# Performance work log

Measured on AMD Instinct MI355X. Metric: run time of the kernel, lower is better.

The kernel has to match this reference:

```python
import jax, jax.numpy as jnp
import numpy as np

N = 50000      # nodes
E = 1600000    # edges (avg degree 32)
IN = 4         # in_size
H = 64         # hidden size


def _gcn_conv(x, W, b, src, dst, ew, n):
    """PyG GCNConv with edge_weight: add self-loops (weight 1), symmetric
    deg^{-1/2} normalization, gather-transform-scatter aggregation, then bias."""
    xw = x @ W  # [n, out] transform first (PyG lin before propagate)
    loops = jnp.arange(n)
    s = jnp.concatenate([src, loops])
    d = jnp.concatenate([dst, loops])
    w = jnp.concatenate([ew, jnp.ones((n,), ew.dtype)])
    deg = jax.ops.segment_sum(w, d, num_segments=n)
    dinv = jnp.where(deg > 0, jax.lax.rsqrt(deg), 0.0)
    norm = dinv[s] * w * dinv[d]                      # [E+n]
    msg = xw[s] * norm[:, None]                       # [E+n, out]
    out = jax.ops.segment_sum(msg, d, num_segments=n)
    return out + b


def _tower(x, src, dst, ew, W0, b0, W1, b1, W2, b2, Wl, bl):
    # basic_gcn: GCNConv+ReLU, GCNConv+ReLU, GCNConv, then nn.Linear(out,out)
    n = x.shape[0]
    h = jax.nn.relu(_gcn_conv(x, W0, b0, src, dst, ew, n))
    h = jax.nn.relu(_gcn_conv(h, W1, b1, src, dst, ew, n))
    h = _gcn_conv(h, W2, b2, src, dst, ew, n)
    return h @ Wl + bl


def setup_inputs() -> dict:
    key = jax.random.key(0)
    ks = jax.random.split(key, 20)
    x = jax.random.normal(ks[0], (N, IN), dtype=jnp.float32)
    edge_index = jax.random.randint(ks[1], (2, E), 0, N, dtype=jnp.int64)
    edge_weights = jax.random.uniform(ks[2], (E,), dtype=jnp.float32)

    def lin(k, fin, fout):
        return jax.random.normal(k, (fin, fout), dtype=jnp.float32) * (1.0 / np.sqrt(fin))

    inp = {"x": x, "edge_index": edge_index, "edge_weights": edge_weights}
    # optim tower: in_size=4 -> 64 -> 64 -> 1, plus Linear(1,1)
    inp["o_W0"], inp["o_b0"] = lin(ks[3], IN, H), jnp.zeros((H,), jnp.float32)
    inp["o_W1"], inp["o_b1"] = lin(ks[4], H, H), jnp.zeros((H,), jnp.float32)
    inp["o_W2"], inp["o_b2"] = lin(ks[5], H, 1), jnp.zeros((1,), jnp.float32)
    inp["o_Wl"], inp["o_bl"] = lin(ks[6], 1, 1), jnp.zeros((1,), jnp.float32)
    # gamma tower: in_size+1=5 -> 64 -> 64 -> 1, plus Linear(1,1)
    inp["g_W0"], inp["g_b0"] = lin(ks[7], IN + 1, H), jnp.zeros((H,), jnp.float32)
    inp["g_W1"], inp["g_b1"] = lin(ks[8], H, H), jnp.zeros((H,), jnp.float32)
    inp["g_W2"], inp["g_b2"] = lin(ks[9], H, 1), jnp.zeros((1,), jnp.float32)
    inp["g_Wl"], inp["g_bl"] = lin(ks[10], 1, 1), jnp.zeros((1,), jnp.float32)
    return inp


def reference(x, edge_index, edge_weights,
              o_W0, o_b0, o_W1, o_b1, o_W2, o_b2, o_Wl, o_bl,
              g_W0, g_b0, g_W1, g_b1, g_W2, g_b2, g_Wl, g_bl):
    src, dst = edge_index[0], edge_index[1]
    # x_sol = optim tower (constraints=None -> no range scaling)
    x_sol = _tower(x, src, dst, edge_weights,
                   o_W0, o_b0, o_W1, o_b1, o_W2, o_b2, o_Wl, o_bl)  # [N,1]
    # gamma tower on cat(x, x_sol[:, -1:]); constraints=[0,1] -> sigmoid scaling
    xin = jnp.concatenate([x, x_sol[:, -1:]], axis=1)               # [N,5]
    g = _tower(xin, src, dst, edge_weights,
               g_W0, g_b0, g_W1, g_b1, g_W2, g_b2, g_Wl, g_bl)      # [N,1]
    gamma = jax.nn.sigmoid(g)  # scale_to_range(x, [0,1])
    # s == g == 1: gated residual combine
    x_new = x[:, -1:] + gamma * (x_sol - x[:, -1:])
    return (x_new, gamma)
```

## Files before the change

kernel.cpp:

```cpp
#include <hip/hip_runtime.h>
#include <hip/hip_fp16.h>
#include <math.h>

#define NN 50000
#define NE 1600000
#define NBK 196
#define EPB 4096
#define CAP 9216

typedef unsigned int u32;
typedef _Float16 f16x8 __attribute__((ext_vector_type(8)));
typedef float f32x4 __attribute__((ext_vector_type(4)));

static inline int cdiv(int a, int b){ return (a + b - 1) / b; }



__global__ void k_bucket(const int* __restrict__ src, const int* __restrict__ dst,
                         const float* __restrict__ ew, int* __restrict__ bcur,
                         int2* __restrict__ seL, int e){
  __shared__ int h[NBK], base[NBK], curL[NBK];
  int t = threadIdx.x;
  for (int b = t; b < NBK; b += 256){ h[b] = 0; curL[b] = 0; }
  __syncthreads();
  int beg = blockIdx.x*EPB;
  int d[16];
  #pragma unroll
  for (int i = 0; i < 16; ++i){
    int idx = beg + t + i*256;
    d[i] = (idx < e) ? dst[idx] : -1;
    if (d[i] >= 0) atomicAdd(&h[d[i] >> 8], 1);
  }
  __syncthreads();
  for (int b = t; b < NBK; b += 256)
    if (h[b] > 0) base[b] = b*CAP + atomicAdd(&bcur[b], h[b]);
  __syncthreads();
  #pragma unroll
  for (int i = 0; i < 16; ++i){
    int idx = beg + t + i*256;
    if (idx >= e) continue;
    int dd = d[i], b = dd >> 8;
    int pos = base[b] + atomicAdd(&curL[b], 1);
    seL[pos] = make_int2(((dd & 255) << 16) | src[idx], __float_as_int(ew[idx]));
  }
}

__global__ void k_csr_bucket(const int* __restrict__ bcur, const int2* __restrict__ seL,
                             const float* __restrict__ x, int* __restrict__ rowS,
                             int* __restrict__ rowE, u32* __restrict__ packed,
                             float* __restrict__ dinv, float* __restrict__ xd, int n){
  __shared__ int2 eb[CAP];
  __shared__ int hist[256], sh[256], cur[256];
  __shared__ float wsum[256];
  int b = blockIdx.x, t = threadIdx.x;
  int cnt = bcur[b];
  int ebeg = b*CAP;
  hist[t] = 0; wsum[t] = 0.f;
  __syncthreads();
  for (int i = t; i < cnt; i += 256){
    int2 u = seL[ebeg + i];
    eb[i] = u;
    int d = u.x >> 16;
    atomicAdd(&hist[d], 1);
    atomicAdd(&wsum[d], __int_as_float(u.y));
  }
  __syncthreads();
  int v = hist[t];
  sh[t] = v; __syncthreads();
  for (int o = 1; o < 256; o <<= 1){
    int u = (t >= o) ? sh[t-o] : 0;
    __syncthreads();
    sh[t] += u;
    __syncthreads();
  }
  int rs = ebeg + sh[t] - v;
  int node = b*256 + t;
  if (node < n){ rowS[node] = rs; rowE[node] = rs + v; }
  cur[t] = rs;
  __syncthreads();
  for (int i = t; i < cnt; i += 256){
    int2 u = eb[i];
    int d = u.x >> 16;
    int pos = atomicAdd(&cur[d], 1);
    packed[pos] = (u32)(u.x & 0xFFFF) |
                  ((u32)__half_as_ushort(__float2half(__int_as_float(u.y))) << 16);
  }
  __syncthreads();
  if (node < n){
    float di = rsqrtf(1.f + wsum[t]);
    dinv[node] = di;
    float4 xv = ((const float4*)x)[node];
    ((float4*)xd)[node] = make_float4(xv.x*di, xv.y*di, xv.z*di, xv.w*di);
  }
}


__global__ void k_agg4(const int* __restrict__ rowS, const int* __restrict__ rowE,
                       const u32* __restrict__ packed, const float* __restrict__ xd,
                       const float* __restrict__ dinv, float* __restrict__ y4, int n){
  int tid = blockIdx.x*256 + threadIdx.x;
  int node = tid >> 2, l = tid & 3;
  if (node >= n) return;
  int p0 = rowS[node] + l, end = rowE[node];
  float ax = 0.f, ay = 0.f, az = 0.f, aw = 0.f;
  auto eproc = [&](int p){
    u32 v = (p < end) ? packed[p] : 0u;
    float w = __half2float(__ushort_as_half((unsigned short)(v >> 16)));
    float4 xs = ((const float4*)xd)[v & 0xFFFF];
    ax = fmaf(w, xs.x, ax);
    ay = fmaf(w, xs.y, ay);
    az = fmaf(w, xs.z, az);
    aw = fmaf(w, xs.w, aw);
  };
  #pragma unroll
  for (int t = 0; t < 12; ++t) eproc(p0 + 4*t);
  for (int p = p0 + 48; p < end; p += 4) eproc(p);
  ax += __shfl_xor(ax, 1, 64);  ax += __shfl_xor(ax, 2, 64);
  ay += __shfl_xor(ay, 1, 64);  ay += __shfl_xor(ay, 2, 64);
  az += __shfl_xor(az, 1, 64);  az += __shfl_xor(az, 2, 64);
  aw += __shfl_xor(aw, 1, 64);  aw += __shfl_xor(aw, 2, 64);
  if (l == 0){
    float4 self = ((const float4*)xd)[node];
    float di = dinv[node];
    ((float4*)y4)[node] = make_float4((ax + self.x)*di, (ay + self.y)*di,
                                      (az + self.z)*di, (aw + self.w)*di);
  }
}

template<int FIN>
__global__ void k_conv2_mfma(const float* __restrict__ y4,
                  const int* __restrict__ rowS, const int* __restrict__ rowE,
                  const u32* __restrict__ packed, const float* __restrict__ xsolh,
                  const float* __restrict__ W0, const float* __restrict__ b0,
                  const float* __restrict__ W1, const float* __restrict__ dinv,
                  __half* __restrict__ out, int n){
  __shared__ float W0s[FIN*64];
  __shared__ float b0s[64];
  int t = threadIdx.x;
  if (t < FIN*64) W0s[t] = W0[t];
  if (t < 64)     b0s[t] = b0[t];
  __syncthreads();

  int lane = t & 63;
  int m = lane & 15, q = lane >> 4;
  int wid = (blockIdx.x*256 + t) >> 6;
  int ntiles = n >> 4;
  if (wid >= ntiles) return;
  int base = wid << 4;

  auto ldB = [&](int kk, int ct){
    f16x8 r;
    #pragma unroll
    for (int j = 0; j < 8; ++j)
      r[j] = (_Float16)W1[(kk*32 + q*8 + j)*64 + ct*16 + m];
    return r;
  };
  f16x8 b00 = ldB(0,0), b01 = ldB(0,1), b02 = ldB(0,2), b03 = ldB(0,3);
  f16x8 b10 = ldB(1,0), b11 = ldB(1,1), b12 = ldB(1,2), b13 = ldB(1,3);

  float4 yv = ((const float4*)y4)[base + m];
  float y5 = 0.f;
  if constexpr (FIN == 5){
    int node = base + m;
    int p0 = rowS[node] + q, end = rowE[node];
    float acc = 0.f;
    auto eproc = [&](int p){
      u32 v = (p < end) ? packed[p] : 0u;
      float w = __half2float(__ushort_as_half((unsigned short)(v >> 16)));
      acc = fmaf(w, xsolh[v & 0xFFFF], acc);
    };
    #pragma unroll
    for (int tt = 0; tt < 8; ++tt) eproc(p0 + 4*tt);
    if (p0 + 32 < end){
      #pragma unroll
      for (int tt = 8; tt < 16; ++tt) eproc(p0 + 4*tt);
    }
    for (int p = p0 + 64; p < end; p += 4) eproc(p);
    acc += __shfl_xor(acc, 16, 64);
    acc += __shfl_xor(acc, 32, 64);
    y5 = (acc + xsolh[node]) * dinv[node];
  }
  f16x8 a0, a1;
  #pragma unroll
  for (int j = 0; j < 8; ++j){
    int c0i = q*8 + j, c1i = 32 + q*8 + j;
    float h0 = b0s[c0i], h1 = b0s[c1i];
    h0 = fmaf(yv.x, W0s[0*64 + c0i], h0);  h1 = fmaf(yv.x, W0s[0*64 + c1i], h1);
    h0 = fmaf(yv.y, W0s[1*64 + c0i], h0);  h1 = fmaf(yv.y, W0s[1*64 + c1i], h1);
    h0 = fmaf(yv.z, W0s[2*64 + c0i], h0);  h1 = fmaf(yv.z, W0s[2*64 + c1i], h1);
    h0 = fmaf(yv.w, W0s[3*64 + c0i], h0);  h1 = fmaf(yv.w, W0s[3*64 + c1i], h1);
    if constexpr (FIN == 5){
      h0 = fmaf(y5, W0s[4*64 + c0i], h0);  h1 = fmaf(y5, W0s[4*64 + c1i], h1);
    }
    a0[j] = (_Float16)fmaxf(h0, 0.f);
    a1[j] = (_Float16)fmaxf(h1, 0.f);
  }
  f32x4 c0 = {0,0,0,0}, c1 = {0,0,0,0}, c2 = {0,0,0,0}, c3 = {0,0,0,0};
  c0 = __builtin_amdgcn_mfma_f32_16x16x32_f16(a0, b00, c0, 0, 0, 0);
  c0 = __builtin_amdgcn_mfma_f32_16x16x32_f16(a1, b10, c0, 0, 0, 0);
  c1 = __builtin_amdgcn_mfma_f32_16x16x32_f16(a0, b01, c1, 0, 0, 0);
  c1 = __builtin_amdgcn_mfma_f32_16x16x32_f16(a1, b11, c1, 0, 0, 0);
  c2 = __builtin_amdgcn_mfma_f32_16x16x32_f16(a0, b02, c2, 0, 0, 0);
  c2 = __builtin_amdgcn_mfma_f32_16x16x32_f16(a1, b12, c2, 0, 0, 0);
  c3 = __builtin_amdgcn_mfma_f32_16x16x32_f16(a0, b03, c3, 0, 0, 0);
  c3 = __builtin_amdgcn_mfma_f32_16x16x32_f16(a1, b13, c3, 0, 0, 0);

  float4 dv = ((const float4*)dinv)[wid*4 + q];
  float dvr[4] = {dv.x, dv.y, dv.z, dv.w};
  auto st = [&](const f32x4& c, int ct){
    int ft = ct*16 + m;
    #pragma unroll
    for (int r = 0; r < 4; ++r)
      out[(size_t)(base + q*4 + r)*64 + ft] = __float2half(c[r]*dvr[r]);
  };
  st(c0, 0); st(c1, 1); st(c2, 2); st(c3, 3);
}

__global__ __attribute__((amdgpu_waves_per_eu(4, 8)))
void k_agg64f(const int* __restrict__ rowS, const int* __restrict__ rowE,
              const u32* __restrict__ packed, const __half* __restrict__ xw,
              const float* __restrict__ dinv, const float* __restrict__ b,
              const float* __restrict__ W2, float* __restrict__ shat, int n){
  int tid = blockIdx.x*256 + threadIdx.x;
  int node = tid >> 6, lane = tid & 63;
  if (node >= n) return;
  int f4 = lane & 15, ep = lane >> 4;
  int ep1 = ep & 1, ep2 = ep & 2;
  const uint2* xw4 = (const uint2*)xw;
  float a0 = 0.f, a1 = 0.f, a2 = 0.f, a3 = 0.f;
  int p = rowS[node], end = rowE[node];

  auto proc = [&](u32 myv, int t){
    u32 w0 = __builtin_amdgcn_readlane(myv, 4*t);
    u32 w1 = __builtin_amdgcn_readlane(myv, 4*t + 1);
    u32 w2 = __builtin_amdgcn_readlane(myv, 4*t + 2);
    u32 w3 = __builtin_amdgcn_readlane(myv, 4*t + 3);
    u32 lo = ep1 ? w1 : w0;
    u32 hi = ep1 ? w3 : w2;
    u32 v = ep2 ? hi : lo;
    int s = v & 0xFFFF;
    float w = __half2float(__ushort_as_half((unsigned short)(v >> 16)));
    uint2 g = xw4[s*16 + f4];
    float2 g0 = __half22float2(*(const __half2*)&g.x);
    float2 g1 = __half22float2(*(const __half2*)&g.y);
    a0 = fmaf(w, g0.x, a0);
    a1 = fmaf(w, g0.y, a1);
    a2 = fmaf(w, g1.x, a2);
    a3 = fmaf(w, g1.y, a3);
  };

  for (; p + 64 <= end; p += 64){
    u32 myv = __builtin_nontemporal_load(&packed[p + lane]);
    #pragma unroll
    for (int t = 0; t < 16; ++t) proc(myv, t);
  }
  int rem = end - p;
  if (rem > 0){
    u32 myv = (lane < rem) ? packed[p + lane] : 0u;
    #pragma unroll
    for (int t = 0; t < 8; ++t) proc(myv, t);
    if (rem > 32){
      #pragma unroll
      for (int t = 8; t < 16; ++t) proc(myv, t);
    }
  }

  a0 += __shfl_xor(a0, 16, 64);  a0 += __shfl_xor(a0, 32, 64);
  a1 += __shfl_xor(a1, 16, 64);  a1 += __shfl_xor(a1, 32, 64);
  a2 += __shfl_xor(a2, 16, 64);  a2 += __shfl_xor(a2, 32, 64);
  a3 += __shfl_xor(a3, 16, 64);  a3 += __shfl_xor(a3, 32, 64);

  float di = dinv[node];
  uint2 gs = xw4[(size_t)node*16 + f4];
  float2 s0 = __half22float2(*(const __half2*)&gs.x);
  float2 s1 = __half22float2(*(const __half2*)&gs.y);
  float4 bb = ((const float4*)b)[f4];
  float4 ww = ((const float4*)W2)[f4];
  float h0 = (a0 + s0.x)*di + bb.x;
  float h1 = (a1 + s0.y)*di + bb.y;
  float h2 = (a2 + s1.x)*di + bb.z;
  float h3 = (a3 + s1.y)*di + bb.w;
  float part = fmaxf(h0, 0.f)*ww.x + fmaxf(h1, 0.f)*ww.y
             + fmaxf(h2, 0.f)*ww.z + fmaxf(h3, 0.f)*ww.w;
  part += __shfl_xor(part, 8, 64);
  part += __shfl_xor(part, 4, 64);
  part += __shfl_xor(part, 2, 64);
  part += __shfl_xor(part, 1, 64);
  if (lane == 0) shat[node] = part * di;
}


__global__ void k_agg1_xsol(const int* __restrict__ rowS, const int* __restrict__ rowE,
                            const u32* __restrict__ packed, const float* __restrict__ shat,
                            const float* __restrict__ dinv, const float* __restrict__ b,
                            const float* __restrict__ Wl, const float* __restrict__ bl,
                            float* __restrict__ xsol, float* __restrict__ xsolh, int n){
  int tid = blockIdx.x*256 + threadIdx.x;
  int node = tid >> 5, l = tid & 31;
  if (node >= n) return;
  int beg = rowS[node], end = rowE[node];
  float acc = 0.f;
  for (int p = beg + l; p < end; p += 32){
    u32 v = packed[p];
    float w = __half2float(__ushort_as_half((unsigned short)(v >> 16)));
    acc = fmaf(w, shat[v & 0xFFFF], acc);
  }
  acc += __shfl_xor(acc, 16, 64);
  acc += __shfl_xor(acc, 8, 64);
  acc += __shfl_xor(acc, 4, 64);
  acc += __shfl_xor(acc, 2, 64);
  acc += __shfl_xor(acc, 1, 64);
  if (l == 0){
    float di = dinv[node];
    float h = (acc + shat[node])*di + b[0];
    float v = h*Wl[0] + bl[0];
    xsol[node]  = v;
    xsolh[node] = v*di;
  }
}

__global__ void k_agg1_final(const int* __restrict__ rowS, const int* __restrict__ rowE,
                             const u32* __restrict__ packed, const float* __restrict__ shat,
                             const float* __restrict__ dinv, const float* __restrict__ b,
                             const float* __restrict__ Wl, const float* __restrict__ bl,
                             const float* __restrict__ xsol, const float* __restrict__ x,
                             float* __restrict__ out, int n){
  int tid = blockIdx.x*256 + threadIdx.x;
  int node = tid >> 5, l = tid & 31;
  if (node >= n) return;
  int beg = rowS[node], end = rowE[node];
  float acc = 0.f;
  for (int p = beg + l; p < end; p += 32){
    u32 v = packed[p];
    float w = __half2float(__ushort_as_half((unsigned short)(v >> 16)));
    acc = fmaf(w, shat[v & 0xFFFF], acc);
  }
  acc += __shfl_xor(acc, 16, 64);
  acc += __shfl_xor(acc, 8, 64);
  acc += __shfl_xor(acc, 4, 64);
  acc += __shfl_xor(acc, 2, 64);
  acc += __shfl_xor(acc, 1, 64);
  if (l == 0){
    float di = dinv[node];
    float g = ((acc + shat[node])*di + b[0])*Wl[0] + bl[0];
    float gamma = 1.f / (1.f + expf(-g));
    float xl = x[node*4+3];
    out[node]     = xl + gamma*(xsol[node] - xl);
    out[n + node] = gamma;
  }
}


extern "C" void kernel_launch(void* const* d_in, const int* in_sizes, int n_in,
                              void* d_out, int out_size, void* d_ws, size_t ws_size,
                              hipStream_t stream){
  const float* x   = (const float*)d_in[0];
  const int*   ei  = (const int*)d_in[1];
  const float* ew  = (const float*)d_in[2];
  const float* oW0 = (const float*)d_in[3];
  const float* ob0 = (const float*)d_in[4];
  const float* oW1 = (const float*)d_in[5];
  const float* ob1 = (const float*)d_in[6];
  const float* oW2 = (const float*)d_in[7];
  const float* ob2 = (const float*)d_in[8];
  const float* oWl = (const float*)d_in[9];
  const float* obl = (const float*)d_in[10];
  const float* gW0 = (const float*)d_in[11];
  const float* gb0 = (const float*)d_in[12];
  const float* gW1 = (const float*)d_in[13];
  const float* gb1 = (const float*)d_in[14];
  const float* gW2 = (const float*)d_in[15];
  const float* gb2 = (const float*)d_in[16];
  const float* gWl = (const float*)d_in[17];
  const float* gbl = (const float*)d_in[18];

  const int n = NN, e = NE;
  const int* src = ei;
  const int* dst = ei + e;

  char* wsb = (char*)d_ws;
  int2*  seL    = (int2*)wsb;      wsb += (size_t)NBK*CAP*sizeof(int2);
  u32*   packed = (u32*)wsb;       wsb += (size_t)NBK*CAP*4;
  __half* bufA  = (__half*)wsb;    wsb += (size_t)n*64*2;
  float* y4     = (float*)wsb;     wsb += (size_t)n*4*4;
  float* xd     = (float*)wsb;     wsb += (size_t)n*4*4;
  int*   rowS   = (int*)wsb;       wsb += (size_t)n*4;
  int*   rowE   = (int*)wsb;       wsb += (size_t)n*4;
  int*   bcur   = (int*)wsb;       wsb += 256*4;
  float* dinv   = (float*)wsb;     wsb += (size_t)n*4;
  float* shat   = (float*)wsb;     wsb += (size_t)n*4;
  float* xsol   = (float*)wsb;     wsb += (size_t)n*4;
  float* xsolh  = (float*)wsb;     wsb += (size_t)n*4;

  dim3 b256(256);
  int gw  = cdiv(n*64, 256);
  int gw2 = cdiv(n*32, 256);
  int gw4 = cdiv(n*4, 256);
  int gb  = cdiv(e, EPB);
  int gxm = cdiv((n >> 4)*64, 256);

  hipMemsetAsync(bcur, 0, 256*4, stream);
  k_bucket    <<<gb,  b256, 0, stream>>>(src, dst, ew, bcur, seL, e);
  k_csr_bucket<<<NBK, b256, 0, stream>>>(bcur, seL, x, rowS, rowE, packed, dinv, xd, n);

  k_agg4      <<<gw4, b256, 0, stream>>>(rowS, rowE, packed, xd, dinv, y4, n);

  k_conv2_mfma<4><<<gxm, b256, 0, stream>>>(y4, rowS, rowE, packed, nullptr,
                                            oW0, ob0, oW1, dinv, bufA, n);
  k_agg64f       <<<gw,  b256, 0, stream>>>(rowS, rowE, packed, bufA, dinv, ob1, oW2, shat, n);
  k_agg1_xsol    <<<gw2, b256, 0, stream>>>(rowS, rowE, packed, shat, dinv, ob2, oWl, obl, xsol, xsolh, n);

  k_conv2_mfma<5><<<gxm, b256, 0, stream>>>(y4, rowS, rowE, packed, xsolh,
                                            gW0, gb0, gW1, dinv, bufA, n);
  k_agg64f       <<<gw,  b256, 0, stream>>>(rowS, rowE, packed, bufA, dinv, gb1, gW2, shat, n);
  k_agg1_final   <<<gw2, b256, 0, stream>>>(rowS, rowE, packed, shat, dinv, gb2, gWl, gbl, xsol, x, (float*)d_out, n);
}
```

Measured before the change: 262.2 us.

## Split 64-wide aggregation into two 32-feature halves for cache locality

The conv2 output is stored as two feature-major halves of 32 features each, and the 64-feature aggregation runs as two passes, one per half. Each pass then gathers from a 3.2 MB table instead of 6.4 MB, so random neighbour gathers are more likely to hit in L2/MALL. The cost is reading the edge list twice, an extra kernel launch per tower, and a small partial-sum buffer. Each lane's gather also shrinks from 8 to 4 bytes.

```diff
diff --git a/kernel.cpp b/kernel.cpp
--- a/kernel.cpp
+++ b/kernel.cpp
@@ -209,25 +209,28 @@
   float dvr[4] = {dv.x, dv.y, dv.z, dv.w};
   auto st = [&](const f32x4& c, int ct){
     int ft = ct*16 + m;
+    size_t hoff = (size_t)(ft >> 5)*(size_t)n*32 + (ft & 31);
     #pragma unroll
     for (int r = 0; r < 4; ++r)
-      out[(size_t)(base + q*4 + r)*64 + ft] = __float2half(c[r]*dvr[r]);
+      out[hoff + (size_t)(base + q*4 + r)*32] = __float2half(c[r]*dvr[r]);
   };
   st(c0, 0); st(c1, 1); st(c2, 2); st(c3, 3);
 }
 
+template<int PHASE>
 __global__ __attribute__((amdgpu_waves_per_eu(4, 8)))
-void k_agg64f(const int* __restrict__ rowS, const int* __restrict__ rowE,
+void k_agg64h(const int* __restrict__ rowS, const int* __restrict__ rowE,
               const u32* __restrict__ packed, const __half* __restrict__ xw,
               const float* __restrict__ dinv, const float* __restrict__ b,
-              const float* __restrict__ W2, float* __restrict__ shat, int n){
+              const float* __restrict__ W2, float* __restrict__ psum,
+              float* __restrict__ shat, int n){
   int tid = blockIdx.x*256 + threadIdx.x;
   int node = tid >> 6, lane = tid & 63;
   if (node >= n) return;
-  int f4 = lane & 15, ep = lane >> 4;
+  int f2 = lane & 15, ep = lane >> 4;
   int ep1 = ep & 1, ep2 = ep & 2;
-  const uint2* xw4 = (const uint2*)xw;
-  float a0 = 0.f, a1 = 0.f, a2 = 0.f, a3 = 0.f;
+  const u32* xh = (const u32*)(xw + (size_t)PHASE*(size_t)n*32);
+  float a0 = 0.f, a1 = 0.f;
   int p = rowS[node], end = rowE[node];
 
   auto proc = [&](u32 myv, int t){
@@ -240,13 +243,10 @@
     u32 v = ep2 ? hi : lo;
     int s = v & 0xFFFF;
     float w = __half2float(__ushort_as_half((unsigned short)(v >> 16)));
-    uint2 g = xw4[s*16 + f4];
-    float2 g0 = __half22float2(*(const __half2*)&g.x);
-    float2 g1 = __half22float2(*(const __half2*)&g.y);
-    a0 = fmaf(w, g0.x, a0);
-    a1 = fmaf(w, g0.y, a1);
-    a2 = fmaf(w, g1.x, a2);
-    a3 = fmaf(w, g1.y, a3);
+    u32 g = xh[s*16 + f2];
+    float2 gf = __half22float2(*(const __half2*)&g);
+    a0 = fmaf(w, gf.x, a0);
+    a1 = fmaf(w, gf.y, a1);
   };
 
   for (; p + 64 <= end; p += 64){
@@ -267,26 +267,23 @@
 
   a0 += __shfl_xor(a0, 16, 64);  a0 += __shfl_xor(a0, 32, 64);
   a1 += __shfl_xor(a1, 16, 64);  a1 += __shfl_xor(a1, 32, 64);
-  a2 += __shfl_xor(a2, 16, 64);  a2 += __shfl_xor(a2, 32, 64);
-  a3 += __shfl_xor(a3, 16, 64);  a3 += __shfl_xor(a3, 32, 64);
 
   float di = dinv[node];
-  uint2 gs = xw4[(size_t)node*16 + f4];
-  float2 s0 = __half22float2(*(const __half2*)&gs.x);
-  float2 s1 = __half22float2(*(const __half2*)&gs.y);
-  float4 bb = ((const float4*)b)[f4];
-  float4 ww = ((const float4*)W2)[f4];
-  float h0 = (a0 + s0.x)*di + bb.x;
-  float h1 = (a1 + s0.y)*di + bb.y;
-  float h2 = (a2 + s1.x)*di + bb.z;
-  float h3 = (a3 + s1.y)*di + bb.w;
-  float part = fmaxf(h0, 0.f)*ww.x + fmaxf(h1, 0.f)*ww.y
-             + fmaxf(h2, 0.f)*ww.z + fmaxf(h3, 0.f)*ww.w;
+  u32 gs = xh[(size_t)node*16 + f2];
+  float2 sf = __half22float2(*(const __half2*)&gs);
+  float2 bb = ((const float2*)b)[PHASE*16 + f2];
+  float2 ww = ((const float2*)W2)[PHASE*16 + f2];
+  float h0 = (a0 + sf.x)*di + bb.x;
+  float h1 = (a1 + sf.y)*di + bb.y;
+  float part = fmaxf(h0, 0.f)*ww.x + fmaxf(h1, 0.f)*ww.y;
   part += __shfl_xor(part, 8, 64);
   part += __shfl_xor(part, 4, 64);
   part += __shfl_xor(part, 2, 64);
   part += __shfl_xor(part, 1, 64);
-  if (lane == 0) shat[node] = part * di;
+  if (lane == 0){
+    if constexpr (PHASE == 0) psum[node] = part;
+    else                      shat[node] = (psum[node] + part) * di;
+  }
 }
 
 
@@ -389,6 +386,7 @@
   int*   bcur   = (int*)wsb;       wsb += 256*4;
   float* dinv   = (float*)wsb;     wsb += (size_t)n*4;
   float* shat   = (float*)wsb;     wsb += (size_t)n*4;
+  float* psum   = (float*)wsb;     wsb += (size_t)n*4;
   float* xsol   = (float*)wsb;     wsb += (size_t)n*4;
   float* xsolh  = (float*)wsb;     wsb += (size_t)n*4;
 
@@ -407,11 +405,13 @@
 
   k_conv2_mfma<4><<<gxm, b256, 0, stream>>>(y4, rowS, rowE, packed, nullptr,
                                             oW0, ob0, oW1, dinv, bufA, n);
-  k_agg64f       <<<gw,  b256, 0, stream>>>(rowS, rowE, packed, bufA, dinv, ob1, oW2, shat, n);
+  k_agg64h<0>    <<<gw,  b256, 0, stream>>>(rowS, rowE, packed, bufA, dinv, ob1, oW2, psum, shat, n);
+  k_agg64h<1>    <<<gw,  b256, 0, stream>>>(rowS, rowE, packed, bufA, dinv, ob1, oW2, psum, shat, n);
   k_agg1_xsol    <<<gw2, b256, 0, stream>>>(rowS, rowE, packed, shat, dinv, ob2, oWl, obl, xsol, xsolh, n);
 
   k_conv2_mfma<5><<<gxm, b256, 0, stream>>>(y4, rowS, rowE, packed, xsolh,
                                             gW0, gb0, gW1, dinv, bufA, n);
-  k_agg64f       <<<gw,  b256, 0, stream>>>(rowS, rowE, packed, bufA, dinv, gb1, gW2, shat, n);
+  k_agg64h<0>    <<<gw,  b256, 0, stream>>>(rowS, rowE, packed, bufA, dinv, gb1, gW2, psum, shat, n);
+  k_agg64h<1>    <<<gw,  b256, 0, stream>>>(rowS, rowE, packed, bufA, dinv, gb1, gW2, psum, shat, n);
   k_agg1_final   <<<gw2, b256, 0, stream>>>(rowS, rowE, packed, shat, dinv, gb2, gWl, gbl, xsol, x, (float*)d_out, n);
 }
```

Result: slower. 307.6 us (+17.3%).
